# Kernel optimization log

Measured on AMD Instinct MI355X. Metric: run time of the kernel, lower is better.

Reference implementation:

```python
import jax, jax.numpy as jnp
import numpy as np

NEG_SLOPE = 0.2  # PyG GATConv default negative_slope


def _gat_layer(x, src, dst, W, a_src, a_dst, b, heads, ch, concat, num_nodes):
    # x: [Nt, Fin]; W: [Fin, heads*ch]; a_src/a_dst: [heads, ch]
    xw = (x @ W).reshape(num_nodes, heads, ch)            # [Nt, H, C]
    alpha_s = jnp.sum(xw * a_src, axis=-1)                # [Nt, H]
    alpha_d = jnp.sum(xw * a_dst, axis=-1)                # [Nt, H]
    e = jax.nn.leaky_relu(alpha_s[src] + alpha_d[dst], NEG_SLOPE)  # [E, H]
    # segment softmax over destination nodes (every node has a self-loop)
    m = jax.lax.stop_gradient(jax.ops.segment_max(e, dst, num_segments=num_nodes))
    ex = jnp.exp(e - m[dst])
    denom = jax.ops.segment_sum(ex, dst, num_segments=num_nodes)
    alpha = ex / (denom[dst] + 1e-16)                     # [E, H]
    out = jax.ops.segment_sum(alpha[:, :, None] * xw[src], dst, num_segments=num_nodes)  # [Nt, H, C]
    out = out.reshape(num_nodes, heads * ch) if concat else out.mean(axis=1)
    return out + b


def setup_inputs() -> dict:
    key = jax.random.key(0)
    ks = jax.random.split(key, 12)
    B, N, IN, HID, H, OUT, E = 2, 10000, 256, 256, 2, 256, 160000
    x = jax.random.normal(ks[0], (B, N, IN), dtype=jnp.float32)
    edge_index = jax.random.randint(ks[1], (2, E), 0, N, dtype=jnp.int32)
    s_in = 1.0 / np.sqrt(IN)
    s_h = 1.0 / np.sqrt(HID)
    s_hh = 1.0 / np.sqrt(HID * H)
    W1 = jax.random.normal(ks[2], (IN, H * HID), dtype=jnp.float32) * s_in
    att_src1 = jax.random.normal(ks[3], (H, HID), dtype=jnp.float32) * s_h
    att_dst1 = jax.random.normal(ks[4], (H, HID), dtype=jnp.float32) * s_h
    b1 = jax.random.normal(ks[5], (H * HID,), dtype=jnp.float32) * 0.01
    W2 = jax.random.normal(ks[6], (H * HID, OUT), dtype=jnp.float32) * s_hh
    att_src2 = jax.random.normal(ks[7], (1, OUT), dtype=jnp.float32) * s_h
    att_dst2 = jax.random.normal(ks[8], (1, OUT), dtype=jnp.float32) * s_h
    b2 = jax.random.normal(ks[9], (OUT,), dtype=jnp.float32) * 0.01
    return {"x": x, "edge_index": edge_index, "W1": W1, "att_src1": att_src1,
            "att_dst1": att_dst1, "b1": b1, "W2": W2, "att_src2": att_src2,
            "att_dst2": att_dst2, "b2": b2}


def reference(x, edge_index, W1, att_src1, att_dst1, b1, W2, att_src2, att_dst2, b2):
    B, N, C = x.shape
    H, HID = att_src1.shape
    OUT = W2.shape[1]
    Nt = B * N
    xf = x.reshape(Nt, C)
    # batch edge index with per-graph node offsets (shared edges across batch)
    offs = (jnp.arange(B, dtype=edge_index.dtype) * N)       # [B]
    ei = (edge_index[:, None, :] + offs[None, :, None]).reshape(2, -1)  # [2, B*E]
    # add self loops (PyG GATConv default)
    loops = jnp.arange(Nt, dtype=edge_index.dtype)
    src = jnp.concatenate([ei[0], loops])
    dst = jnp.concatenate([ei[1], loops])
    h = _gat_layer(xf, src, dst, W1, att_src1, att_dst1, b1, H, HID, True, Nt)
    h = jax.nn.gelu(h, approximate=False)  # torch F.gelu default = exact erf
    out = _gat_layer(h, src, dst, W2, att_src2, att_dst2, b2, 1, OUT, False, Nt)
    return out.reshape(B, N, OUT)
```

## Files before the change

### kernel.cpp

```cpp
#include <hip/hip_runtime.h>
#include <math.h>

constexpr int B_   = 2;
constexpr int N_   = 10000;
constexpr int IN_  = 256;
constexpr int HID_ = 256;
constexpr int H1_  = 2;
constexpr int OUT_ = 256;
constexpr int E_   = 160000;
constexpr int NT_  = B_ * N_;
constexpr float SLOPE = 0.2f;
constexpr int DMAX = 128;

typedef unsigned short u16;
typedef __attribute__((ext_vector_type(8))) short short8;
typedef __attribute__((ext_vector_type(4))) float f32x4;

__device__ __forceinline__ u16 f2bf(float f) {
    unsigned int u = __float_as_uint(f);
    u += 0x7fffu + ((u >> 16) & 1u);
    return (u16)(u >> 16);
}
__device__ __forceinline__ void bf8(uint4 r, float4& lo, float4& hi) {
    lo = make_float4(__uint_as_float((r.x & 0xffffu) << 16),
                     __uint_as_float(r.x & 0xffff0000u),
                     __uint_as_float((r.y & 0xffffu) << 16),
                     __uint_as_float(r.y & 0xffff0000u));
    hi = make_float4(__uint_as_float((r.z & 0xffffu) << 16),
                     __uint_as_float(r.z & 0xffff0000u),
                     __uint_as_float((r.w & 0xffffu) << 16),
                     __uint_as_float(r.w & 0xffff0000u));
}
__device__ __forceinline__ void fma4(float4& a, float s, float4 v) {
    a.x = fmaf(s, v.x, a.x); a.y = fmaf(s, v.y, a.y);
    a.z = fmaf(s, v.z, a.z); a.w = fmaf(s, v.w, a.w);
}
__device__ __forceinline__ float lrelu(float e) { return (e < 0.f) ? SLOPE * e : e; }

__device__ __forceinline__ void g2l16(const void* g, void* l) {
    __builtin_amdgcn_global_load_lds(
        (const __attribute__((address_space(1))) unsigned int*)g,
        (__attribute__((address_space(3))) unsigned int*)l, 16, 0, 0);
}

__global__ __launch_bounds__(256) void k_wprep(
    const float* __restrict__ W1,
    const float* __restrict__ aS1, const float* __restrict__ aD1,
    const float* __restrict__ W2,
    const float* __restrict__ aS2, const float* __restrict__ aD2,
    float* __restrict__ w1s, float* __restrict__ w1d,
    float* __restrict__ w2s, float* __restrict__ w2d,
    u16* __restrict__ W1t, u16* __restrict__ W2t,
    uint4* __restrict__ zbase) {
    __shared__ float tld[32][33];
    const int blk = blockIdx.x;
    if (blk < 16) {
        for (int i = blk * 256 + threadIdx.x; i < 12500; i += 16 * 256)
            zbase[i] = make_uint4(0, 0, 0, 0);
    } else if (blk < 528) {
        int wv = (blk - 16) * 4 + (threadIdx.x >> 6);
        int lane = threadIdx.x & 63;
        int c = lane * 4;
        float4 wr, av;
        if (wv < 1024) {
            int h = (wv >> 8) & 1;
            int k = wv & 255;
            const float* a = (wv < 512) ? aS1 : aD1;
            wr = *(const float4*)(W1 + (size_t)k * 512 + h * 256 + c);
            av = *(const float4*)(a + h * 256 + c);
        } else {
            int k = (wv - 1024) & 511;
            const float* a = (wv < 1536) ? aS2 : aD2;
            wr = *(const float4*)(W2 + (size_t)k * 256 + c);
            av = *(const float4*)(a + c);
        }
        float s = wr.x * av.x + wr.y * av.y + wr.z * av.z + wr.w * av.w;
        #pragma unroll
        for (int off = 32; off; off >>= 1) s += __shfl_down(s, off);
        if (lane == 0) {
            if (wv < 512)       w1s[wv] = s;
            else if (wv < 1024) w1d[wv - 512] = s;
            else if (wv < 1536) w2s[wv - 1024] = s;
            else                w2d[wv - 1536] = s;
        }
    } else {
        const int b = blk - 528;
        const int z = b >> 7;
        const int bb = b & 127;
        const float* S = z ? W2 : W1;
        u16* D = z ? W2t : W1t;
        const int R = z ? 512 : 256;
        const int C = z ? 256 : 512;
        const int xt = C >> 5;
        const int bx = bb % xt, by = bb / xt;
        const int tx = threadIdx.x & 31, ty = threadIdx.x >> 5;
        int xx = bx * 32 + tx;
        int y0 = by * 32 + ty;
        #pragma unroll
        for (int i = 0; i < 32; i += 8)
            tld[ty + i][tx] = S[(size_t)(y0 + i) * C + xx];
        __syncthreads();
        int xo = by * 32 + tx;
        int yo = bx * 32 + ty;
        #pragma unroll
        for (int i = 0; i < 32; i += 8)
            D[(size_t)(yo + i) * R + xo] = f2bf(tld[tx][ty + i]);
    }
}

__global__ __launch_bounds__(256) void k_pre(
    const float* __restrict__ x, u16* __restrict__ Xb,
    const float* __restrict__ w1s, const float* __restrict__ w1d,
    float* __restrict__ as1, float* __restrict__ ad1,
    const int* __restrict__ ei, int* __restrict__ cnt, int* __restrict__ bucket) {
    const int NB = NT_ / 4;
    if ((int)blockIdx.x < NB) {
        const int w = threadIdx.x >> 6, lane = threadIdx.x & 63;
        const int nt = blockIdx.x * 4 + w;
        const int c = lane * 4;
        float4 v = *(const float4*)(x + (size_t)nt * 256 + c);
        ((uint2*)(Xb + (size_t)nt * 256))[lane] =
            make_uint2((unsigned)f2bf(v.x) | ((unsigned)f2bf(v.y) << 16),
                       (unsigned)f2bf(v.z) | ((unsigned)f2bf(v.w) << 16));
        float4 s0v = *(const float4*)(w1s + c);
        float4 s1v = *(const float4*)(w1s + 256 + c);
        float4 d0v = *(const float4*)(w1d + c);
        float4 d1v = *(const float4*)(w1d + 256 + c);
        float s0 = v.x*s0v.x + v.y*s0v.y + v.z*s0v.z + v.w*s0v.w;
        float s1 = v.x*s1v.x + v.y*s1v.y + v.z*s1v.z + v.w*s1v.w;
        float d0 = v.x*d0v.x + v.y*d0v.y + v.z*d0v.z + v.w*d0v.w;
        float d1 = v.x*d1v.x + v.y*d1v.y + v.z*d1v.z + v.w*d1v.w;
        #pragma unroll
        for (int off = 32; off; off >>= 1) {
            s0 += __shfl_down(s0, off); s1 += __shfl_down(s1, off);
            d0 += __shfl_down(d0, off); d1 += __shfl_down(d1, off);
        }
        if (lane == 0) {
            as1[nt * 2] = s0; as1[nt * 2 + 1] = s1;
            ad1[nt * 2] = d0; ad1[nt * 2 + 1] = d1;
        }
    } else {
        int e = (blockIdx.x - NB) * 256 + threadIdx.x;
        if (e < E_) {
            int s = ei[e], d = ei[E_ + e];
            int p = atomicAdd(&cnt[d], 1);
            if (p < DMAX - 1) bucket[d * DMAX + p] = s;
        }
    }
}

__global__ __launch_bounds__(256) void k_agg1x(
    const u16* __restrict__ Xb,
    const float* __restrict__ as_, const float* __restrict__ ad_,
    const int* __restrict__ cnt, const int* __restrict__ bucket,
    u16* __restrict__ Y) {
    __shared__ int   stl[4][DMAX];
    __shared__ float exw[4][2 * DMAX];
    const int w    = threadIdx.x >> 6;
    const int lane = threadIdx.x & 63;
    const int half = lane >> 5;
    const int l32  = lane & 31;
    const int nt   = blockIdx.x * 4 + w;
    if (nt >= NT_) return;
    const int nl   = nt % N_;
    const int boff = nt - nl;
    const int r0   = nl * DMAX;
    int deg = cnt[nl]; deg = (deg < DMAX - 1) ? deg : (DMAX - 1);
    const float adv0 = ad_[nt * 2], adv1 = ad_[nt * 2 + 1];
    const float adv = half ? adv1 : adv0;

    for (int i = lane; i <= deg; i += 64)
        stl[w][i] = (i < deg) ? (bucket[r0 + i] + boff) : nt;

    float den = 0.f;
    for (int i = l32; i <= deg; i += 32) {
        int st = stl[w][i];
        float ex = __expf(lrelu(as_[st * 2 + half] + adv));
        exw[w][2 * i + half] = ex;
        den += ex;
    }
    #pragma unroll
    for (int off = 16; off; off >>= 1) den += __shfl_xor(den, off);
    const float inv = 1.f / (den + 1e-16f);
    const float invO = __shfl_xor(inv, 32);

    const int slot = half;
    const int nin = deg + 1;
    const u16* fb = Xb + l32 * 8;
    float4 A0l = {0,0,0,0}, A0h = {0,0,0,0}, A1l = {0,0,0,0}, A1h = {0,0,0,0};
    float4 B0l = {0,0,0,0}, B0h = {0,0,0,0}, B1l = {0,0,0,0}, B1h = {0,0,0,0};
    int j = 0;
    for (; j + 8 <= nin; j += 8) {
        int sA = stl[w][j + slot],     sB = stl[w][j + 2 + slot];
        int sC = stl[w][j + 4 + slot], sD = stl[w][j + 6 + slot];
        float2 wA = *(const float2*)&exw[w][2 * (j + slot)];
        float2 wB = *(const float2*)&exw[w][2 * (j + 2 + slot)];
        float2 wC = *(const float2*)&exw[w][2 * (j + 4 + slot)];
        float2 wD = *(const float2*)&exw[w][2 * (j + 6 + slot)];
        uint4 vA = *(const uint4*)(fb + (size_t)sA * 256);
        uint4 vB = *(const uint4*)(fb + (size_t)sB * 256);
        uint4 vC = *(const uint4*)(fb + (size_t)sC * 256);
        uint4 vD = *(const uint4*)(fb + (size_t)sD * 256);
        float4 lo, hi;
        bf8(vA, lo, hi); fma4(A0l, wA.x, lo); fma4(A0h, wA.x, hi);
                         fma4(A1l, wA.y, lo); fma4(A1h, wA.y, hi);
        bf8(vB, lo, hi); fma4(B0l, wB.x, lo); fma4(B0h, wB.x, hi);
                         fma4(B1l, wB.y, lo); fma4(B1h, wB.y, hi);
        bf8(vC, lo, hi); fma4(A0l, wC.x, lo); fma4(A0h, wC.x, hi);
                         fma4(A1l, wC.y, lo); fma4(A1h, wC.y, hi);
        bf8(vD, lo, hi); fma4(B0l, wD.x, lo); fma4(B0h, wD.x, hi);
                         fma4(B1l, wD.y, lo); fma4(B1h, wD.y, hi);
    }
    for (int jj = j + slot; jj < nin; jj += 2) {
        int s0 = stl[w][jj];
        float2 w01 = *(const float2*)&exw[w][2 * jj];
        uint4 v0 = *(const uint4*)(fb + (size_t)s0 * 256);
        float4 lo, hi;
        bf8(v0, lo, hi); fma4(A0l, w01.x, lo); fma4(A0h, w01.x, hi);
                         fma4(A1l, w01.y, lo); fma4(A1h, w01.y, hi);
    }
    A0l.x += B0l.x; A0l.y += B0l.y; A0l.z += B0l.z; A0l.w += B0l.w;
    A0h.x += B0h.x; A0h.y += B0h.y; A0h.z += B0h.z; A0h.w += B0h.w;
    A1l.x += B1l.x; A1l.y += B1l.y; A1l.z += B1l.z; A1l.w += B1l.w;
    A1h.x += B1h.x; A1h.y += B1h.y; A1h.z += B1h.z; A1h.w += B1h.w;
    A0l.x += __shfl_xor(A0l.x, 32); A0l.y += __shfl_xor(A0l.y, 32);
    A0l.z += __shfl_xor(A0l.z, 32); A0l.w += __shfl_xor(A0l.w, 32);
    A0h.x += __shfl_xor(A0h.x, 32); A0h.y += __shfl_xor(A0h.y, 32);
    A0h.z += __shfl_xor(A0h.z, 32); A0h.w += __shfl_xor(A0h.w, 32);
    A1l.x += __shfl_xor(A1l.x, 32); A1l.y += __shfl_xor(A1l.y, 32);
    A1l.z += __shfl_xor(A1l.z, 32); A1l.w += __shfl_xor(A1l.w, 32);
    A1h.x += __shfl_xor(A1h.x, 32); A1h.y += __shfl_xor(A1h.y, 32);
    A1h.w += __shfl_xor(A1h.w, 32); A1h.z += __shfl_xor(A1h.z, 32);

    if (slot == 0) {
        float f0[8] = { A0l.x*inv,  A0l.y*inv,  A0l.z*inv,  A0l.w*inv,
                        A0h.x*inv,  A0h.y*inv,  A0h.z*inv,  A0h.w*inv };
        float f1[8] = { A1l.x*invO, A1l.y*invO, A1l.z*invO, A1l.w*invO,
                        A1h.x*invO, A1h.y*invO, A1h.z*invO, A1h.w*invO };
        size_t ob = (size_t)nt * 512 + l32 * 8;
        *(uint4*)(Y + ob) =
            make_uint4((unsigned)f2bf(f0[0]) | ((unsigned)f2bf(f0[1]) << 16),
                       (unsigned)f2bf(f0[2]) | ((unsigned)f2bf(f0[3]) << 16),
                       (unsigned)f2bf(f0[4]) | ((unsigned)f2bf(f0[5]) << 16),
                       (unsigned)f2bf(f0[6]) | ((unsigned)f2bf(f0[7]) << 16));
        *(uint4*)(Y + ob + 256) =
            make_uint4((unsigned)f2bf(f1[0]) | ((unsigned)f2bf(f1[1]) << 16),
                       (unsigned)f2bf(f1[2]) | ((unsigned)f2bf(f1[3]) << 16),
                       (unsigned)f2bf(f1[4]) | ((unsigned)f2bf(f1[5]) << 16),
                       (unsigned)f2bf(f1[6]) | ((unsigned)f2bf(f1[7]) << 16));
    }
}

__global__ __launch_bounds__(256, 6) void gemm_g(
    const u16* __restrict__ Yf, const u16* __restrict__ W1t,
    u16* __restrict__ Hb,
    const float* __restrict__ b1,
    const float* __restrict__ w2s, const float* __restrict__ w2d,
    float* __restrict__ as2, float* __restrict__ ad2, int M) {
    __shared__ u16 sA[64 * 64], sB[64 * 64];
    const int tid = threadIdx.x, wave = tid >> 6, lane = tid & 63;
    const int bm = blockIdx.x, bn = blockIdx.y, h = blockIdx.z;

    const int rsel = lane >> 3;
    const int kc   = ((lane & 7) ^ rsel) * 8;
    int rA0 = bm * 64 + wave * 16 + rsel;
    int rA1 = rA0 + 8;
    rA0 = (rA0 < M) ? rA0 : (M - 1);
    rA1 = (rA1 < M) ? rA1 : (M - 1);
    const int rB = bn * 64 + wave * 16 + rsel;
    const u16* gA0 = Yf + (size_t)rA0 * 512 + h * 256 + kc;
    const u16* gA1 = Yf + (size_t)rA1 * 512 + h * 256 + kc;
    const u16* gB0 = W1t + (size_t)(h * 256 + rB) * 256 + kc;
    const u16* gB1 = W1t + (size_t)(h * 256 + rB + 8) * 256 + kc;
    u16* lA0 = sA + wave * 1024; u16* lA1 = lA0 + 512;
    u16* lB0 = sB + wave * 1024; u16* lB1 = lB0 + 512;

    const int wm = wave & 1, wn = wave >> 1;
    const int l15 = lane & 15, quad = lane >> 4;
    const int sw  = l15 & 7;
    const int aR0 = (wm * 32 + l15) * 64; const int aR1 = aR0 + 1024;
    const int bR0 = (wn * 32 + l15) * 64; const int bR1 = bR0 + 1024;
    const int c0 = (quad ^ sw) * 8;
    const int c1 = ((4 + quad) ^ sw) * 8;

    f32x4 acc[2][2];
    #pragma unroll
    for (int i = 0; i < 2; i++)
        #pragma unroll
        for (int j = 0; j < 2; j++)
            acc[i][j] = (f32x4){0.f, 0.f, 0.f, 0.f};

    for (int k0 = 0; k0 < 256; k0 += 64) {
        g2l16(gA0 + k0, lA0); g2l16(gA1 + k0, lA1);
        g2l16(gB0 + k0, lB0); g2l16(gB1 + k0, lB1);
        __syncthreads();
        short8 a0 = *(const short8*)(sA + aR0 + c0);
        short8 a1 = *(const short8*)(sA + aR1 + c0);
        short8 b0 = *(const short8*)(sB + bR0 + c0);
        short8 b1v = *(const short8*)(sB + bR1 + c0);
        acc[0][0] = __builtin_amdgcn_mfma_f32_16x16x32_bf16(a0, b0, acc[0][0], 0, 0, 0);
        acc[0][1] = __builtin_amdgcn_mfma_f32_16x16x32_bf16(a0, b1v, acc[0][1], 0, 0, 0);
        acc[1][0] = __builtin_amdgcn_mfma_f32_16x16x32_bf16(a1, b0, acc[1][0], 0, 0, 0);
        acc[1][1] = __builtin_amdgcn_mfma_f32_16x16x32_bf16(a1, b1v, acc[1][1], 0, 0, 0);
        a0 = *(const short8*)(sA + aR0 + c1);
        a1 = *(const short8*)(sA + aR1 + c1);
        b0 = *(const short8*)(sB + bR0 + c1);
        b1v = *(const short8*)(sB + bR1 + c1);
        acc[0][0] = __builtin_amdgcn_mfma_f32_16x16x32_bf16(a0, b0, acc[0][0], 0, 0, 0);
        acc[0][1] = __builtin_amdgcn_mfma_f32_16x16x32_bf16(a0, b1v, acc[0][1], 0, 0, 0);
        acc[1][0] = __builtin_amdgcn_mfma_f32_16x16x32_bf16(a1, b0, acc[1][0], 0, 0, 0);
        acc[1][1] = __builtin_amdgcn_mfma_f32_16x16x32_bf16(a1, b1v, acc[1][1], 0, 0, 0);
        __syncthreads();
    }

    const int colL = bn * 64 + wn * 32;
    float Bv[2], Sv[2], Dv[2];
    #pragma unroll
    for (int j = 0; j < 2; j++) {
        int cg = h * 256 + colL + j * 16 + l15;
        Bv[j] = b1[cg]; Sv[j] = w2s[cg]; Dv[j] = w2d[cg];
    }
    #pragma unroll
    for (int i = 0; i < 2; i++) {
        #pragma unroll
        for (int r = 0; r < 4; r++) {
            int row = bm * 64 + wm * 32 + i * 16 + quad * 4 + r;
            float o[2], ps = 0.f, pd = 0.f;
            #pragma unroll
            for (int j = 0; j < 2; j++) {
                float v = acc[i][j][r] + Bv[j];
                v = 0.5f * v * (1.f + erff(v * 0.70710678118654752f));
                o[j] = v;
                ps = fmaf(v, Sv[j], ps);
                pd = fmaf(v, Dv[j], pd);
            }
            #pragma unroll
            for (int off = 1; off < 16; off <<= 1) {
                ps += __shfl_xor(ps, off);
                pd += __shfl_xor(pd, off);
            }
            if (row < M) {
                if (l15 == 0) { atomicAdd(&as2[row], ps); atomicAdd(&ad2[row], pd); }
                #pragma unroll
                for (int j = 0; j < 2; j++)
                    Hb[(size_t)row * 512 + h * 256 + colL + j * 16 + l15] = f2bf(o[j]);
            }
        }
    }
}

__global__ __launch_bounds__(256, 6) void gemm_p(
    const u16* __restrict__ A, const u16* __restrict__ Bt,
    u16* __restrict__ C16, int M, int N, int K) {
    __shared__ u16 sA[64 * 64], sB[64 * 64];
    const int tid = threadIdx.x, wave = tid >> 6, lane = tid & 63;
    const int bm = blockIdx.x, bn = blockIdx.y;

    const int rsel = lane >> 3;
    const int kc   = ((lane & 7) ^ rsel) * 8;
    int rA0 = bm * 64 + wave * 16 + rsel;
    int rA1 = rA0 + 8;
    rA0 = (rA0 < M) ? rA0 : (M - 1);
    rA1 = (rA1 < M) ? rA1 : (M - 1);
    const int rB = bn * 64 + wave * 16 + rsel;
    const u16* gA0 = A + (size_t)rA0 * K + kc;
    const u16* gA1 = A + (size_t)rA1 * K + kc;
    const u16* gB0 = Bt + (size_t)rB * K + kc;
    const u16* gB1 = Bt + (size_t)(rB + 8) * K + kc;
    u16* lA0 = sA + wave * 1024; u16* lA1 = lA0 + 512;
    u16* lB0 = sB + wave * 1024; u16* lB1 = lB0 + 512;

    const int wm = wave & 1, wn = wave >> 1;
    const int l15 = lane & 15, quad = lane >> 4;
    const int sw  = l15 & 7;
    const int aR0 = (wm * 32 + l15) * 64; const int aR1 = aR0 + 1024;
    const int bR0 = (wn * 32 + l15) * 64; const int bR1 = bR0 + 1024;
    const int c0 = (quad ^ sw) * 8;
    const int c1 = ((4 + quad) ^ sw) * 8;

    f32x4 acc[2][2];
    #pragma unroll
    for (int i = 0; i < 2; i++)
        #pragma unroll
        for (int j = 0; j < 2; j++)
            acc[i][j] = (f32x4){0.f, 0.f, 0.f, 0.f};

    for (int k0 = 0; k0 < K; k0 += 64) {
        g2l16(gA0 + k0, lA0); g2l16(gA1 + k0, lA1);
        g2l16(gB0 + k0, lB0); g2l16(gB1 + k0, lB1);
        __syncthreads();
        short8 a0 = *(const short8*)(sA + aR0 + c0);
        short8 a1 = *(const short8*)(sA + aR1 + c0);
        short8 b0 = *(const short8*)(sB + bR0 + c0);
        short8 b1v = *(const short8*)(sB + bR1 + c0);
        acc[0][0] = __builtin_amdgcn_mfma_f32_16x16x32_bf16(a0, b0, acc[0][0], 0, 0, 0);
        acc[0][1] = __builtin_amdgcn_mfma_f32_16x16x32_bf16(a0, b1v, acc[0][1], 0, 0, 0);
        acc[1][0] = __builtin_amdgcn_mfma_f32_16x16x32_bf16(a1, b0, acc[1][0], 0, 0, 0);
        acc[1][1] = __builtin_amdgcn_mfma_f32_16x16x32_bf16(a1, b1v, acc[1][1], 0, 0, 0);
        a0 = *(const short8*)(sA + aR0 + c1);
        a1 = *(const short8*)(sA + aR1 + c1);
        b0 = *(const short8*)(sB + bR0 + c1);
        b1v = *(const short8*)(sB + bR1 + c1);
        acc[0][0] = __builtin_amdgcn_mfma_f32_16x16x32_bf16(a0, b0, acc[0][0], 0, 0, 0);
        acc[0][1] = __builtin_amdgcn_mfma_f32_16x16x32_bf16(a0, b1v, acc[0][1], 0, 0, 0);
        acc[1][0] = __builtin_amdgcn_mfma_f32_16x16x32_bf16(a1, b0, acc[1][0], 0, 0, 0);
        acc[1][1] = __builtin_amdgcn_mfma_f32_16x16x32_bf16(a1, b1v, acc[1][1], 0, 0, 0);
        __syncthreads();
    }
    #pragma unroll
    for (int i = 0; i < 2; i++) {
        #pragma unroll
        for (int r = 0; r < 4; r++) {
            int row = bm * 64 + wm * 32 + i * 16 + quad * 4 + r;
            if (row < M) {
                #pragma unroll
                for (int j = 0; j < 2; j++) {
                    int col = bn * 64 + wn * 32 + j * 16 + l15;
                    C16[(size_t)row * N + col] = f2bf(acc[i][j][r]);
                }
            }
        }
    }
}

__global__ __launch_bounds__(256) void k_agg_h1(
    const u16* __restrict__ feat,
    const float* __restrict__ as_, const float* __restrict__ ad_,
    const int* __restrict__ cnt, const int* __restrict__ bucket,
    const float* __restrict__ bias,
    float* __restrict__ out) {
    __shared__ int   stl[4][DMAX];
    __shared__ float exw[4][DMAX];
    const int w    = threadIdx.x >> 6;
    const int lane = threadIdx.x & 63;
    const int slot = lane >> 5;
    const int l32  = lane & 31;
    const int nt   = blockIdx.x * 4 + w;
    if (nt >= NT_) return;
    const int nl   = nt % N_;
    const int boff = nt - nl;
    const int r0   = nl * DMAX;
    int deg = cnt[nl]; deg = (deg < DMAX - 1) ? deg : (DMAX - 1);
    const float adv = ad_[nt];

    for (int i = lane; i <= deg; i += 64)
        stl[w][i] = (i < deg) ? (bucket[r0 + i] + boff) : nt;

    float den = 0.f;
    for (int i = lane; i <= deg; i += 64) {
        int st = stl[w][i];
        float ex = __expf(lrelu(as_[st] + adv));
        exw[w][i] = ex;
        den += ex;
    }
    #pragma unroll
    for (int off = 32; off; off >>= 1) den += __shfl_xor(den, off);
    const float inv = 1.f / (den + 1e-16f);

    const int nin = deg + 1;
    const u16* fb = feat + l32 * 8;
    float4 aA0 = {0,0,0,0}, aB0 = {0,0,0,0}, aA1 = {0,0,0,0}, aB1 = {0,0,0,0};
    int j = 0;
    for (; j + 8 <= nin; j += 8) {
        int sA = stl[w][j + slot],     sB = stl[w][j + 2 + slot];
        int sC = stl[w][j + 4 + slot], sD = stl[w][j + 6 + slot];
        float wA = exw[w][j + slot],     wB = exw[w][j + 2 + slot];
        float wC = exw[w][j + 4 + slot], wD = exw[w][j + 6 + slot];
        uint4 vA = *(const uint4*)(fb + (size_t)sA * 256);
        uint4 vB = *(const uint4*)(fb + (size_t)sB * 256);
        uint4 vC = *(const uint4*)(fb + (size_t)sC * 256);
        uint4 vD = *(const uint4*)(fb + (size_t)sD * 256);
        float4 lo, hi;
        bf8(vA, lo, hi); fma4(aA0, wA, lo); fma4(aB0, wA, hi);
        bf8(vB, lo, hi); fma4(aA1, wB, lo); fma4(aB1, wB, hi);
        bf8(vC, lo, hi); fma4(aA0, wC, lo); fma4(aB0, wC, hi);
        bf8(vD, lo, hi); fma4(aA1, wD, lo); fma4(aB1, wD, hi);
    }
    for (; j + 4 <= nin; j += 4) {
        int sA = stl[w][j + slot], sB = stl[w][j + 2 + slot];
        float wA = exw[w][j + slot], wB = exw[w][j + 2 + slot];
        uint4 vA = *(const uint4*)(fb + (size_t)sA * 256);
        uint4 vB = *(const uint4*)(fb + (size_t)sB * 256);
        float4 lo, hi;
        bf8(vA, lo, hi); fma4(aA0, wA, lo); fma4(aB0, wA, hi);
        bf8(vB, lo, hi); fma4(aA1, wB, lo); fma4(aB1, wB, hi);
    }
    for (int jj = j + slot; jj < nin; jj += 2) {
        int s0 = stl[w][jj];
        float w0 = exw[w][jj];
        uint4 v0 = *(const uint4*)(fb + (size_t)s0 * 256);
        float4 lo, hi;
        bf8(v0, lo, hi); fma4(aA0, w0, lo); fma4(aB0, w0, hi);
    }
    aA0.x += aA1.x; aA0.y += aA1.y; aA0.z += aA1.z; aA0.w += aA1.w;
    aB0.x += aB1.x; aB0.y += aB1.y; aB0.z += aB1.z; aB0.w += aB1.w;
    aA0.x += __shfl_xor(aA0.x, 32); aA0.y += __shfl_xor(aA0.y, 32);
    aA0.z += __shfl_xor(aA0.z, 32); aA0.w += __shfl_xor(aA0.w, 32);
    aB0.x += __shfl_xor(aB0.x, 32); aB0.y += __shfl_xor(aB0.y, 32);
    aB0.z += __shfl_xor(aB0.z, 32); aB0.w += __shfl_xor(aB0.w, 32);

    if (slot == 0) {
        int c = l32 * 8;
        float4 b0 = *(const float4*)(bias + c);
        float4 b1 = *(const float4*)(bias + c + 4);
        float* ob = out + (size_t)nt * 256 + c;
        *(float4*)(ob)     = make_float4(aA0.x * inv + b0.x, aA0.y * inv + b0.y,
                                         aA0.z * inv + b0.z, aA0.w * inv + b0.w);
        *(float4*)(ob + 4) = make_float4(aB0.x * inv + b1.x, aB0.y * inv + b1.y,
                                         aB0.z * inv + b1.z, aB0.w * inv + b1.w);
    }
}

extern "C" void kernel_launch(void* const* d_in, const int* in_sizes, int n_in,
                              void* d_out, int out_size, void* d_ws, size_t ws_size,
                              hipStream_t stream) {
    const float* x    = (const float*)d_in[0];
    const int*   ei   = (const int*)  d_in[1];
    const float* W1   = (const float*)d_in[2];
    const float* aS1  = (const float*)d_in[3];
    const float* aD1  = (const float*)d_in[4];
    const float* b1   = (const float*)d_in[5];
    const float* W2   = (const float*)d_in[6];
    const float* aS2  = (const float*)d_in[7];
    const float* aD2  = (const float*)d_in[8];
    const float* b2   = (const float*)d_in[9];
    float* out = (float*)d_out;

    u16* Xb   = (u16*)d_ws;
    u16* Y    = Xb + (size_t)NT_ * 256;
    u16* Hb   = Y  + (size_t)NT_ * 512;
    u16* hw16 = Hb + (size_t)NT_ * 512;
    float* as1 = (float*)(hw16 + (size_t)NT_ * 256);
    float* ad1 = as1 + NT_ * H1_;
    float* as2 = ad1 + NT_ * H1_;
    float* ad2 = as2 + NT_;
    int* cnt   = (int*)(ad2 + NT_);
    int* bucket= cnt + N_;
    u16* W1t   = (u16*)(bucket + N_ * DMAX);
    u16* W2t   = W1t + 512 * 256;
    float* w1s = (float*)(W2t + 256 * 512);
    float* w1d = w1s + 512;
    float* w2s = w1d + 512;
    float* w2d = w2s + 512;

    k_wprep<<<784, 256, 0, stream>>>(W1, aS1, aD1, W2, aS2, aD2,
                                     w1s, w1d, w2s, w2d, W1t, W2t, (uint4*)as2);

    k_pre<<<NT_ / 4 + (E_ + 255) / 256, 256, 0, stream>>>(
        x, Xb, w1s, w1d, as1, ad1, ei, cnt, bucket);

    k_agg1x<<<(NT_ + 3) / 4, 256, 0, stream>>>(Xb, as1, ad1, cnt, bucket, Y);
    gemm_g<<<dim3((NT_ + 63) / 64, 4, 2), 256, 0, stream>>>(
        Y, W1t, Hb, b1, w2s, w2d, as2, ad2, NT_);

    gemm_p<<<dim3((NT_ + 63) / 64, OUT_ / 64), 256, 0, stream>>>(
        Hb, W2t, hw16, NT_, OUT_, H1_ * HID_);
    k_agg_h1<<<(NT_ + 3) / 4, 256, 0, stream>>>(hw16, as2, ad2, cnt, bucket, b2, out);
}
```

Measured before the change: 187.5 us.

## Double-buffer LDS tiles in the bf16 GEMM kernels to overlap loads with MFMA

Both MFMA GEMM kernels now use two LDS buffers for A and B. The next K-tile is staged while the current one is computed, which halves the barriers per iteration and hides global-to-LDS latency. gemm_g is fully unrolled for its four K-tiles. gemm_p loops two tiles at a time and assumes an even tile count. The doubled shared memory lowers the launch-bounds occupancy hint from 6 to 5 blocks, and a shuffle line is reordered cosmetically.

```diff
diff --git a/kernel.cpp b/kernel.cpp
--- a/kernel.cpp
+++ b/kernel.cpp
@@ -230,7 +230,7 @@
     A1l.x += __shfl_xor(A1l.x, 32); A1l.y += __shfl_xor(A1l.y, 32);
     A1l.z += __shfl_xor(A1l.z, 32); A1l.w += __shfl_xor(A1l.w, 32);
     A1h.x += __shfl_xor(A1h.x, 32); A1h.y += __shfl_xor(A1h.y, 32);
-    A1h.w += __shfl_xor(A1h.w, 32); A1h.z += __shfl_xor(A1h.z, 32);
+    A1h.z += __shfl_xor(A1h.z, 32); A1h.w += __shfl_xor(A1h.w, 32);
 
     if (slot == 0) {
         float f0[8] = { A0l.x*inv,  A0l.y*inv,  A0l.z*inv,  A0l.w*inv,
@@ -251,13 +251,13 @@
     }
 }
 
-__global__ __launch_bounds__(256, 6) void gemm_g(
+__global__ __launch_bounds__(256, 5) void gemm_g(
     const u16* __restrict__ Yf, const u16* __restrict__ W1t,
     u16* __restrict__ Hb,
     const float* __restrict__ b1,
     const float* __restrict__ w2s, const float* __restrict__ w2d,
     float* __restrict__ as2, float* __restrict__ ad2, int M) {
-    __shared__ u16 sA[64 * 64], sB[64 * 64];
+    __shared__ u16 sA[2][64 * 64], sB[2][64 * 64];
     const int tid = threadIdx.x, wave = tid >> 6, lane = tid & 63;
     const int bm = blockIdx.x, bn = blockIdx.y, h = blockIdx.z;
 
@@ -272,8 +272,7 @@
     const u16* gA1 = Yf + (size_t)rA1 * 512 + h * 256 + kc;
     const u16* gB0 = W1t + (size_t)(h * 256 + rB) * 256 + kc;
     const u16* gB1 = W1t + (size_t)(h * 256 + rB + 8) * 256 + kc;
-    u16* lA0 = sA + wave * 1024; u16* lA1 = lA0 + 512;
-    u16* lB0 = sB + wave * 1024; u16* lB1 = lB0 + 512;
+    const int lofs = wave * 1024;
 
     const int wm = wave & 1, wn = wave >> 1;
     const int l15 = lane & 15, quad = lane >> 4;
@@ -290,28 +289,35 @@
         for (int j = 0; j < 2; j++)
             acc[i][j] = (f32x4){0.f, 0.f, 0.f, 0.f};
 
-    for (int k0 = 0; k0 < 256; k0 += 64) {
-        g2l16(gA0 + k0, lA0); g2l16(gA1 + k0, lA1);
-        g2l16(gB0 + k0, lB0); g2l16(gB1 + k0, lB1);
-        __syncthreads();
-        short8 a0 = *(const short8*)(sA + aR0 + c0);
-        short8 a1 = *(const short8*)(sA + aR1 + c0);
-        short8 b0 = *(const short8*)(sB + bR0 + c0);
-        short8 b1v = *(const short8*)(sB + bR1 + c0);
+    auto stage = [&](int k0, int b) {
+        g2l16(gA0 + k0, &sA[b][lofs]);       g2l16(gA1 + k0, &sA[b][lofs + 512]);
+        g2l16(gB0 + k0, &sB[b][lofs]);       g2l16(gB1 + k0, &sB[b][lofs + 512]);
+    };
+    auto compute = [&](const u16* A_, const u16* B_) {
+        short8 a0 = *(const short8*)(A_ + aR0 + c0);
+        short8 a1 = *(const short8*)(A_ + aR1 + c0);
+        short8 b0 = *(const short8*)(B_ + bR0 + c0);
+        short8 b1v = *(const short8*)(B_ + bR1 + c0);
         acc[0][0] = __builtin_amdgcn_mfma_f32_16x16x32_bf16(a0, b0, acc[0][0], 0, 0, 0);
         acc[0][1] = __builtin_amdgcn_mfma_f32_16x16x32_bf16(a0, b1v, acc[0][1], 0, 0, 0);
         acc[1][0] = __builtin_amdgcn_mfma_f32_16x16x32_bf16(a1, b0, acc[1][0], 0, 0, 0);
         acc[1][1] = __builtin_amdgcn_mfma_f32_16x16x32_bf16(a1, b1v, acc[1][1], 0, 0, 0);
-        a0 = *(const short8*)(sA + aR0 + c1);
-        a1 = *(const short8*)(sA + aR1 + c1);
-        b0 = *(const short8*)(sB + bR0 + c1);
-        b1v = *(const short8*)(sB + bR1 + c1);
+        a0 = *(const short8*)(A_ + aR0 + c1);
+        a1 = *(const short8*)(A_ + aR1 + c1);
+        b0 = *(const short8*)(B_ + bR0 + c1);
+        b1v = *(const short8*)(B_ + bR1 + c1);
         acc[0][0] = __builtin_amdgcn_mfma_f32_16x16x32_bf16(a0, b0, acc[0][0], 0, 0, 0);
         acc[0][1] = __builtin_amdgcn_mfma_f32_16x16x32_bf16(a0, b1v, acc[0][1], 0, 0, 0);
         acc[1][0] = __builtin_amdgcn_mfma_f32_16x16x32_bf16(a1, b0, acc[1][0], 0, 0, 0);
         acc[1][1] = __builtin_amdgcn_mfma_f32_16x16x32_bf16(a1, b1v, acc[1][1], 0, 0, 0);
-        __syncthreads();
-    }
+    };
+
+    stage(0, 0);
+    __syncthreads();
+    stage(64, 1);  compute(sA[0], sB[0]); __syncthreads();
+    stage(128, 0); compute(sA[1], sB[1]); __syncthreads();
+    stage(192, 1); compute(sA[0], sB[0]); __syncthreads();
+                   compute(sA[1], sB[1]);
 
     const int colL = bn * 64 + wn * 32;
     float Bv[2], Sv[2], Dv[2];
@@ -349,10 +355,10 @@
     }
 }
 
-__global__ __launch_bounds__(256, 6) void gemm_p(
+__global__ __launch_bounds__(256, 5) void gemm_p(
     const u16* __restrict__ A, const u16* __restrict__ Bt,
     u16* __restrict__ C16, int M, int N, int K) {
-    __shared__ u16 sA[64 * 64], sB[64 * 64];
+    __shared__ u16 sA[2][64 * 64], sB[2][64 * 64];
     const int tid = threadIdx.x, wave = tid >> 6, lane = tid & 63;
     const int bm = blockIdx.x, bn = blockIdx.y;
 
@@ -367,8 +373,7 @@
     const u16* gA1 = A + (size_t)rA1 * K + kc;
     const u16* gB0 = Bt + (size_t)rB * K + kc;
     const u16* gB1 = Bt + (size_t)(rB + 8) * K + kc;
-    u16* lA0 = sA + wave * 1024; u16* lA1 = lA0 + 512;
-    u16* lB0 = sB + wave * 1024; u16* lB1 = lB0 + 512;
+    const int lofs = wave * 1024;
 
     const int wm = wave & 1, wn = wave >> 1;
     const int l15 = lane & 15, quad = lane >> 4;
@@ -385,28 +390,41 @@
         for (int j = 0; j < 2; j++)
             acc[i][j] = (f32x4){0.f, 0.f, 0.f, 0.f};
 
-    for (int k0 = 0; k0 < K; k0 += 64) {
-        g2l16(gA0 + k0, lA0); g2l16(gA1 + k0, lA1);
-        g2l16(gB0 + k0, lB0); g2l16(gB1 + k0, lB1);
-        __syncthreads();
-        short8 a0 = *(const short8*)(sA + aR0 + c0);
-        short8 a1 = *(const short8*)(sA + aR1 + c0);
-        short8 b0 = *(const short8*)(sB + bR0 + c0);
-        short8 b1v = *(const short8*)(sB + bR1 + c0);
+    auto stage = [&](int k0, int b) {
+        g2l16(gA0 + k0, &sA[b][lofs]);       g2l16(gA1 + k0, &sA[b][lofs + 512]);
+        g2l16(gB0 + k0, &sB[b][lofs]);       g2l16(gB1 + k0, &sB[b][lofs + 512]);
+    };
+    auto compute = [&](const u16* A_, const u16* B_) {
+        short8 a0 = *(const short8*)(A_ + aR0 + c0);
+        short8 a1 = *(const short8*)(A_ + aR1 + c0);
+        short8 b0 = *(const short8*)(B_ + bR0 + c0);
+        short8 b1v = *(const short8*)(B_ + bR1 + c0);
         acc[0][0] = __builtin_amdgcn_mfma_f32_16x16x32_bf16(a0, b0, acc[0][0], 0, 0, 0);
         acc[0][1] = __builtin_amdgcn_mfma_f32_16x16x32_bf16(a0, b1v, acc[0][1], 0, 0, 0);
         acc[1][0] = __builtin_amdgcn_mfma_f32_16x16x32_bf16(a1, b0, acc[1][0], 0, 0, 0);
         acc[1][1] = __builtin_amdgcn_mfma_f32_16x16x32_bf16(a1, b1v, acc[1][1], 0, 0, 0);
-        a0 = *(const short8*)(sA + aR0 + c1);
-        a1 = *(const short8*)(sA + aR1 + c1);
-        b0 = *(const short8*)(sB + bR0 + c1);
-        b1v = *(const short8*)(sB + bR1 + c1);
+        a0 = *(const short8*)(A_ + aR0 + c1);
+        a1 = *(const short8*)(A_ + aR1 + c1);
+        b0 = *(const short8*)(B_ + bR0 + c1);
+        b1v = *(const short8*)(B_ + bR1 + c1);
         acc[0][0] = __builtin_amdgcn_mfma_f32_16x16x32_bf16(a0, b0, acc[0][0], 0, 0, 0);
         acc[0][1] = __builtin_amdgcn_mfma_f32_16x16x32_bf16(a0, b1v, acc[0][1], 0, 0, 0);
         acc[1][0] = __builtin_amdgcn_mfma_f32_16x16x32_bf16(a1, b0, acc[1][0], 0, 0, 0);
         acc[1][1] = __builtin_amdgcn_mfma_f32_16x16x32_bf16(a1, b1v, acc[1][1], 0, 0, 0);
+    };
+
+    const int nt = K >> 6;
+    stage(0, 0);
+    __syncthreads();
+    for (int t = 0; t < nt; t += 2) {
+        if (t + 1 < nt) stage((t + 1) << 6, 1);
+        compute(sA[0], sB[0]);
         __syncthreads();
-    }
+        if (t + 2 < nt) stage((t + 2) << 6, 0);
+        compute(sA[1], sB[1]);
+        __syncthreads();
+    }
+
     #pragma unroll
     for (int i = 0; i < 2; i++) {
         #pragma unroll
```

Measured after the change: 193.2 us. +3.0%, slower.

## Make GEMMs persistent with resident B tile and double-buffered A staging

Applied to the files above, without the earlier changes.

Both GEMM kernels become persistent: each block loads its full weight (B) slice into LDS once, then loops over many M tiles, double-buffering A tiles so the next k-chunk loads while MFMAs run on the current one. The goal is to stop reloading the weight tile for every output tile and to overlap global-to-LDS traffic with compute. The costs are a much larger LDS footprint, lower occupancy (launch bounds drop to 3 and 2), and fixed grids of 64x4x2 and 128x4 blocks that may underfill or unevenly load the GPU.

```diff
diff --git a/kernel.cpp b/kernel.cpp
--- a/kernel.cpp
+++ b/kernel.cpp
@@ -11,6 +11,7 @@
 constexpr int NT_  = B_ * N_;
 constexpr float SLOPE = 0.2f;
 constexpr int DMAX = 128;
+constexpr int MT_  = (NT_ + 63) / 64;
 
 typedef unsigned short u16;
 typedef __attribute__((ext_vector_type(8))) short short8;
@@ -230,7 +231,7 @@
     A1l.x += __shfl_xor(A1l.x, 32); A1l.y += __shfl_xor(A1l.y, 32);
     A1l.z += __shfl_xor(A1l.z, 32); A1l.w += __shfl_xor(A1l.w, 32);
     A1h.x += __shfl_xor(A1h.x, 32); A1h.y += __shfl_xor(A1h.y, 32);
-    A1h.w += __shfl_xor(A1h.w, 32); A1h.z += __shfl_xor(A1h.z, 32);
+    A1h.z += __shfl_xor(A1h.z, 32); A1h.w += __shfl_xor(A1h.w, 32);
 
     if (slot == 0) {
         float f0[8] = { A0l.x*inv,  A0l.y*inv,  A0l.z*inv,  A0l.w*inv,
@@ -251,37 +252,47 @@
     }
 }
 
-__global__ __launch_bounds__(256, 6) void gemm_g(
+__global__ __launch_bounds__(256, 3) void gemm_g(
     const u16* __restrict__ Yf, const u16* __restrict__ W1t,
     u16* __restrict__ Hb,
     const float* __restrict__ b1,
     const float* __restrict__ w2s, const float* __restrict__ w2d,
     float* __restrict__ as2, float* __restrict__ ad2, int M) {
-    __shared__ u16 sA[64 * 64], sB[64 * 64];
+    __shared__ u16 sB[64 * 256];
+    __shared__ u16 sA[2][64 * 64];
     const int tid = threadIdx.x, wave = tid >> 6, lane = tid & 63;
     const int bm = blockIdx.x, bn = blockIdx.y, h = blockIdx.z;
-
-    const int rsel = lane >> 3;
-    const int kc   = ((lane & 7) ^ rsel) * 8;
-    int rA0 = bm * 64 + wave * 16 + rsel;
-    int rA1 = rA0 + 8;
-    rA0 = (rA0 < M) ? rA0 : (M - 1);
-    rA1 = (rA1 < M) ? rA1 : (M - 1);
-    const int rB = bn * 64 + wave * 16 + rsel;
-    const u16* gA0 = Yf + (size_t)rA0 * 512 + h * 256 + kc;
-    const u16* gA1 = Yf + (size_t)rA1 * 512 + h * 256 + kc;
-    const u16* gB0 = W1t + (size_t)(h * 256 + rB) * 256 + kc;
-    const u16* gB1 = W1t + (size_t)(h * 256 + rB + 8) * 256 + kc;
-    u16* lA0 = sA + wave * 1024; u16* lA1 = lA0 + 512;
-    u16* lB0 = sB + wave * 1024; u16* lB1 = lB0 + 512;
-
     const int wm = wave & 1, wn = wave >> 1;
     const int l15 = lane & 15, quad = lane >> 4;
-    const int sw  = l15 & 7;
-    const int aR0 = (wm * 32 + l15) * 64; const int aR1 = aR0 + 1024;
-    const int bR0 = (wn * 32 + l15) * 64; const int bR1 = bR0 + 1024;
-    const int c0 = (quad ^ sw) * 8;
-    const int c1 = ((4 + quad) ^ sw) * 8;
+
+    {
+        const int rl = lane >> 5;
+        const int u  = lane & 31;
+        #pragma unroll
+        for (int i = 0; i < 8; i++) {
+            int r  = wave * 16 + i * 2 + rl;
+            int us = (u & ~7) | ((u & 7) ^ (r & 7));
+            g2l16(W1t + (size_t)(h * 256 + bn * 64 + r) * 256 + us * 8,
+                  &sB[(wave * 16 + i * 2) * 256]);
+        }
+    }
+
+    const int arl = lane >> 3;
+    const int au  = lane & 7;
+    const int aus = au ^ arl;
+    auto stageA = [&](int tm, int kb, int b) {
+        #pragma unroll
+        for (int i = 0; i < 2; i++) {
+            int R0 = wave * 16 + i * 8;
+            int rg = tm * 64 + R0 + arl;
+            rg = (rg < M) ? rg : (M - 1);
+            g2l16(Yf + (size_t)rg * 512 + h * 256 + kb * 64 + aus * 8,
+                  &sA[b][R0 * 64]);
+        }
+    };
+
+    const int rA0 = wm * 32 + l15, rA1 = rA0 + 16;
+    const int rB0 = wn * 32 + l15, rB1 = rB0 + 16;
 
     f32x4 acc[2][2];
     #pragma unroll
@@ -289,29 +300,6 @@
         #pragma unroll
         for (int j = 0; j < 2; j++)
             acc[i][j] = (f32x4){0.f, 0.f, 0.f, 0.f};
-
-    for (int k0 = 0; k0 < 256; k0 += 64) {
-        g2l16(gA0 + k0, lA0); g2l16(gA1 + k0, lA1);
-        g2l16(gB0 + k0, lB0); g2l16(gB1 + k0, lB1);
-        __syncthreads();
-        short8 a0 = *(const short8*)(sA + aR0 + c0);
-        short8 a1 = *(const short8*)(sA + aR1 + c0);
-        short8 b0 = *(const short8*)(sB + bR0 + c0);
-        short8 b1v = *(const short8*)(sB + bR1 + c0);
-        acc[0][0] = __builtin_amdgcn_mfma_f32_16x16x32_bf16(a0, b0, acc[0][0], 0, 0, 0);
-        acc[0][1] = __builtin_amdgcn_mfma_f32_16x16x32_bf16(a0, b1v, acc[0][1], 0, 0, 0);
-        acc[1][0] = __builtin_amdgcn_mfma_f32_16x16x32_bf16(a1, b0, acc[1][0], 0, 0, 0);
-        acc[1][1] = __builtin_amdgcn_mfma_f32_16x16x32_bf16(a1, b1v, acc[1][1], 0, 0, 0);
-        a0 = *(const short8*)(sA + aR0 + c1);
-        a1 = *(const short8*)(sA + aR1 + c1);
-        b0 = *(const short8*)(sB + bR0 + c1);
-        b1v = *(const short8*)(sB + bR1 + c1);
-        acc[0][0] = __builtin_amdgcn_mfma_f32_16x16x32_bf16(a0, b0, acc[0][0], 0, 0, 0);
-        acc[0][1] = __builtin_amdgcn_mfma_f32_16x16x32_bf16(a0, b1v, acc[0][1], 0, 0, 0);
-        acc[1][0] = __builtin_amdgcn_mfma_f32_16x16x32_bf16(a1, b0, acc[1][0], 0, 0, 0);
-        acc[1][1] = __builtin_amdgcn_mfma_f32_16x16x32_bf16(a1, b1v, acc[1][1], 0, 0, 0);
-        __syncthreads();
-    }
 
     const int colL = bn * 64 + wn * 32;
     float Bv[2], Sv[2], Dv[2];
@@ -320,63 +308,106 @@
         int cg = h * 256 + colL + j * 16 + l15;
         Bv[j] = b1[cg]; Sv[j] = w2s[cg]; Dv[j] = w2d[cg];
     }
-    #pragma unroll
-    for (int i = 0; i < 2; i++) {
-        #pragma unroll
-        for (int r = 0; r < 4; r++) {
-            int row = bm * 64 + wm * 32 + i * 16 + quad * 4 + r;
-            float o[2], ps = 0.f, pd = 0.f;
+
+    stageA(bm, 0, 0);
+    __syncthreads();
+    int buf = 0;
+    for (int t = bm; t < MT_; t += 64) {
+        #pragma unroll
+        for (int kb = 0; kb < 4; kb++) {
+            int nkb = (kb + 1) & 3;
+            int ntl = (kb == 3) ? t + 64 : t;
+            if (ntl < MT_) stageA(ntl, nkb, buf ^ 1);
             #pragma unroll
-            for (int j = 0; j < 2; j++) {
-                float v = acc[i][j][r] + Bv[j];
-                v = 0.5f * v * (1.f + erff(v * 0.70710678118654752f));
-                o[j] = v;
-                ps = fmaf(v, Sv[j], ps);
-                pd = fmaf(v, Dv[j], pd);
+            for (int ks = 0; ks < 2; ks++) {
+                int ua = ks * 4 + quad;
+                short8 a0 = *(const short8*)(&sA[buf][rA0 * 64 + (ua ^ (rA0 & 7)) * 8]);
+                short8 a1 = *(const short8*)(&sA[buf][rA1 * 64 + (ua ^ (rA1 & 7)) * 8]);
+                int vb = kb * 8 + ks * 4 + quad;
+                short8 b0 = *(const short8*)(&sB[rB0 * 256 + ((vb & ~7) | ((vb & 7) ^ (rB0 & 7))) * 8]);
+                short8 b1v = *(const short8*)(&sB[rB1 * 256 + ((vb & ~7) | ((vb & 7) ^ (rB1 & 7))) * 8]);
+                acc[0][0] = __builtin_amdgcn_mfma_f32_16x16x32_bf16(a0, b0, acc[0][0], 0, 0, 0);
+                acc[0][1] = __builtin_amdgcn_mfma_f32_16x16x32_bf16(a0, b1v, acc[0][1], 0, 0, 0);
+                acc[1][0] = __builtin_amdgcn_mfma_f32_16x16x32_bf16(a1, b0, acc[1][0], 0, 0, 0);
+                acc[1][1] = __builtin_amdgcn_mfma_f32_16x16x32_bf16(a1, b1v, acc[1][1], 0, 0, 0);
             }
-            #pragma unroll
-            for (int off = 1; off < 16; off <<= 1) {
-                ps += __shfl_xor(ps, off);
-                pd += __shfl_xor(pd, off);
+            if (kb == 3) {
+                #pragma unroll
+                for (int i = 0; i < 2; i++) {
+                    #pragma unroll
+                    for (int r = 0; r < 4; r++) {
+                        int row = t * 64 + wm * 32 + i * 16 + quad * 4 + r;
+                        float o[2], ps = 0.f, pd = 0.f;
+                        #pragma unroll
+                        for (int j = 0; j < 2; j++) {
+                            float v = acc[i][j][r] + Bv[j];
+                            v = 0.5f * v * (1.f + erff(v * 0.70710678118654752f));
+                            o[j] = v;
+                            ps = fmaf(v, Sv[j], ps);
+                            pd = fmaf(v, Dv[j], pd);
+                        }
+                        #pragma unroll
+                        for (int off = 1; off < 16; off <<= 1) {
+                            ps += __shfl_xor(ps, off);
+                            pd += __shfl_xor(pd, off);
+                        }
+                        if (row < M) {
+                            if (l15 == 0) { atomicAdd(&as2[row], ps); atomicAdd(&ad2[row], pd); }
+                            #pragma unroll
+                            for (int j = 0; j < 2; j++)
+                                Hb[(size_t)row * 512 + h * 256 + colL + j * 16 + l15] = f2bf(o[j]);
+                        }
+                    }
+                }
+                #pragma unroll
+                for (int i = 0; i < 2; i++)
+                    #pragma unroll
+                    for (int j = 0; j < 2; j++)
+                        acc[i][j] = (f32x4){0.f, 0.f, 0.f, 0.f};
             }
-            if (row < M) {
-                if (l15 == 0) { atomicAdd(&as2[row], ps); atomicAdd(&ad2[row], pd); }
-                #pragma unroll
-                for (int j = 0; j < 2; j++)
-                    Hb[(size_t)row * 512 + h * 256 + colL + j * 16 + l15] = f2bf(o[j]);
-            }
-        }
-    }
-}
-
-__global__ __launch_bounds__(256, 6) void gemm_p(
+            __syncthreads();
+            buf ^= 1;
+        }
+    }
+}
+
+__global__ __launch_bounds__(256, 2) void gemm_p(
     const u16* __restrict__ A, const u16* __restrict__ Bt,
-    u16* __restrict__ C16, int M, int N, int K) {
-    __shared__ u16 sA[64 * 64], sB[64 * 64];
+    u16* __restrict__ C16, int M) {
+    __shared__ u16 sB[64 * 512];
+    __shared__ u16 sA[2][64 * 64];
     const int tid = threadIdx.x, wave = tid >> 6, lane = tid & 63;
     const int bm = blockIdx.x, bn = blockIdx.y;
-
-    const int rsel = lane >> 3;
-    const int kc   = ((lane & 7) ^ rsel) * 8;
-    int rA0 = bm * 64 + wave * 16 + rsel;
-    int rA1 = rA0 + 8;
-    rA0 = (rA0 < M) ? rA0 : (M - 1);
-    rA1 = (rA1 < M) ? rA1 : (M - 1);
-    const int rB = bn * 64 + wave * 16 + rsel;
-    const u16* gA0 = A + (size_t)rA0 * K + kc;
-    const u16* gA1 = A + (size_t)rA1 * K + kc;
-    const u16* gB0 = Bt + (size_t)rB * K + kc;
-    const u16* gB1 = Bt + (size_t)(rB + 8) * K + kc;
-    u16* lA0 = sA + wave * 1024; u16* lA1 = lA0 + 512;
-    u16* lB0 = sB + wave * 1024; u16* lB1 = lB0 + 512;
-
     const int wm = wave & 1, wn = wave >> 1;
     const int l15 = lane & 15, quad = lane >> 4;
-    const int sw  = l15 & 7;
-    const int aR0 = (wm * 32 + l15) * 64; const int aR1 = aR0 + 1024;
-    const int bR0 = (wn * 32 + l15) * 64; const int bR1 = bR0 + 1024;
-    const int c0 = (quad ^ sw) * 8;
-    const int c1 = ((4 + quad) ^ sw) * 8;
+
+    {
+        const int u = lane;
+        #pragma unroll
+        for (int i = 0; i < 16; i++) {
+            int r  = wave * 16 + i;
+            int us = (u & ~7) | ((u & 7) ^ (r & 7));
+            g2l16(Bt + (size_t)(bn * 64 + r) * 512 + us * 8,
+                  &sB[r * 512]);
+        }
+    }
+
+    const int arl = lane >> 3;
+    const int au  = lane & 7;
+    const int aus = au ^ arl;
+    auto stageA = [&](int tm, int kb, int b) {
+        #pragma unroll
+        for (int i = 0; i < 2; i++) {
+            int R0 = wave * 16 + i * 8;
+            int rg = tm * 64 + R0 + arl;
+            rg = (rg < M) ? rg : (M - 1);
+            g2l16(A + (size_t)rg * 512 + kb * 64 + aus * 8,
+                  &sA[b][R0 * 64]);
+        }
+    };
+
+    const int rA0 = wm * 32 + l15, rA1 = rA0 + 16;
+    const int rB0 = wn * 32 + l15, rB1 = rB0 + 16;
 
     f32x4 acc[2][2];
     #pragma unroll
@@ -385,40 +416,51 @@
         for (int j = 0; j < 2; j++)
             acc[i][j] = (f32x4){0.f, 0.f, 0.f, 0.f};
 
-    for (int k0 = 0; k0 < K; k0 += 64) {
-        g2l16(gA0 + k0, lA0); g2l16(gA1 + k0, lA1);
-        g2l16(gB0 + k0, lB0); g2l16(gB1 + k0, lB1);
-        __syncthreads();
-        short8 a0 = *(const short8*)(sA + aR0 + c0);
-        short8 a1 = *(const short8*)(sA + aR1 + c0);
-        short8 b0 = *(const short8*)(sB + bR0 + c0);
-        short8 b1v = *(const short8*)(sB + bR1 + c0);
-        acc[0][0] = __builtin_amdgcn_mfma_f32_16x16x32_bf16(a0, b0, acc[0][0], 0, 0, 0);
-        acc[0][1] = __builtin_amdgcn_mfma_f32_16x16x32_bf16(a0, b1v, acc[0][1], 0, 0, 0);
-        acc[1][0] = __builtin_amdgcn_mfma_f32_16x16x32_bf16(a1, b0, acc[1][0], 0, 0, 0);
-        acc[1][1] = __builtin_amdgcn_mfma_f32_16x16x32_bf16(a1, b1v, acc[1][1], 0, 0, 0);
-        a0 = *(const short8*)(sA + aR0 + c1);
-        a1 = *(const short8*)(sA + aR1 + c1);
-        b0 = *(const short8*)(sB + bR0 + c1);
-        b1v = *(const short8*)(sB + bR1 + c1);
-        acc[0][0] = __builtin_amdgcn_mfma_f32_16x16x32_bf16(a0, b0, acc[0][0], 0, 0, 0);
-        acc[0][1] = __builtin_amdgcn_mfma_f32_16x16x32_bf16(a0, b1v, acc[0][1], 0, 0, 0);
-        acc[1][0] = __builtin_amdgcn_mfma_f32_16x16x32_bf16(a1, b0, acc[1][0], 0, 0, 0);
-        acc[1][1] = __builtin_amdgcn_mfma_f32_16x16x32_bf16(a1, b1v, acc[1][1], 0, 0, 0);
-        __syncthreads();
-    }
-    #pragma unroll
-    for (int i = 0; i < 2; i++) {
-        #pragma unroll
-        for (int r = 0; r < 4; r++) {
-            int row = bm * 64 + wm * 32 + i * 16 + quad * 4 + r;
-            if (row < M) {
+    stageA(bm, 0, 0);
+    __syncthreads();
+    int buf = 0;
+    for (int t = bm; t < MT_; t += 128) {
+        #pragma unroll
+        for (int kb = 0; kb < 8; kb++) {
+            int nkb = (kb + 1) & 7;
+            int ntl = (kb == 7) ? t + 128 : t;
+            if (ntl < MT_) stageA(ntl, nkb, buf ^ 1);
+            #pragma unroll
+            for (int ks = 0; ks < 2; ks++) {
+                int ua = ks * 4 + quad;
+                short8 a0 = *(const short8*)(&sA[buf][rA0 * 64 + (ua ^ (rA0 & 7)) * 8]);
+                short8 a1 = *(const short8*)(&sA[buf][rA1 * 64 + (ua ^ (rA1 & 7)) * 8]);
+                int vb = kb * 8 + ks * 4 + quad;
+                short8 b0 = *(const short8*)(&sB[rB0 * 512 + ((vb & ~7) | ((vb & 7) ^ (rB0 & 7))) * 8]);
+                short8 b1v = *(const short8*)(&sB[rB1 * 512 + ((vb & ~7) | ((vb & 7) ^ (rB1 & 7))) * 8]);
+                acc[0][0] = __builtin_amdgcn_mfma_f32_16x16x32_bf16(a0, b0, acc[0][0], 0, 0, 0);
+                acc[0][1] = __builtin_amdgcn_mfma_f32_16x16x32_bf16(a0, b1v, acc[0][1], 0, 0, 0);
+                acc[1][0] = __builtin_amdgcn_mfma_f32_16x16x32_bf16(a1, b0, acc[1][0], 0, 0, 0);
+                acc[1][1] = __builtin_amdgcn_mfma_f32_16x16x32_bf16(a1, b1v, acc[1][1], 0, 0, 0);
+            }
+            if (kb == 7) {
                 #pragma unroll
-                for (int j = 0; j < 2; j++) {
-                    int col = bn * 64 + wn * 32 + j * 16 + l15;
-                    C16[(size_t)row * N + col] = f2bf(acc[i][j][r]);
+                for (int i = 0; i < 2; i++) {
+                    #pragma unroll
+                    for (int r = 0; r < 4; r++) {
+                        int row = t * 64 + wm * 32 + i * 16 + quad * 4 + r;
+                        if (row < M) {
+                            #pragma unroll
+                            for (int j = 0; j < 2; j++) {
+                                int col = bn * 64 + wn * 32 + j * 16 + l15;
+                                C16[(size_t)row * 256 + col] = f2bf(acc[i][j][r]);
+                            }
+                        }
+                    }
                 }
+                #pragma unroll
+                for (int i = 0; i < 2; i++)
+                    #pragma unroll
+                    for (int j = 0; j < 2; j++)
+                        acc[i][j] = (f32x4){0.f, 0.f, 0.f, 0.f};
             }
+            __syncthreads();
+            buf ^= 1;
         }
     }
 }
@@ -550,10 +592,9 @@
         x, Xb, w1s, w1d, as1, ad1, ei, cnt, bucket);
 
     k_agg1x<<<(NT_ + 3) / 4, 256, 0, stream>>>(Xb, as1, ad1, cnt, bucket, Y);
-    gemm_g<<<dim3((NT_ + 63) / 64, 4, 2), 256, 0, stream>>>(
+    gemm_g<<<dim3(64, 4, 2), 256, 0, stream>>>(
         Y, W1t, Hb, b1, w2s, w2d, as2, ad2, NT_);
 
-    gemm_p<<<dim3((NT_ + 63) / 64, OUT_ / 64), 256, 0, stream>>>(
-        Hb, W2t, hw16, NT_, OUT_, H1_ * HID_);
+    gemm_p<<<dim3(128, 4), 256, 0, stream>>>(Hb, W2t, hw16, NT_);
     k_agg_h1<<<(NT_ + 3) / 4, 256, 0, stream>>>(hw16, as2, ad2, cnt, bucket, b2, out);
 }
```

New measurement: 190.5 us. About the same (+1.6%).
